# Kernel optimization log

Measured on AMD Instinct MI355X. Metric: run time of the kernel, lower is better.

The kernel has to match this reference:

```python
import jax, jax.numpy as jnp
import numpy as np

B, H, W, C = 4, 64, 64, 128  # input feature map; num_heads == filters == C


def setup_inputs() -> dict:
    key = jax.random.key(0)
    ks = jax.random.split(key, 5)
    x = jax.random.normal(ks[0], (B, H, W, C), dtype=jnp.float32)
    scale = 0.02  # keep QK^T logits in a sane range for softmax
    Wf = jax.random.normal(ks[1], (C, C), dtype=jnp.float32) * scale
    Wg = jax.random.normal(ks[2], (C, C), dtype=jnp.float32) * scale
    Wh = jax.random.normal(ks[3], (C, C), dtype=jnp.float32) * scale
    Wv = jax.random.normal(ks[4], (C, C), dtype=jnp.float32) * scale
    zeros = jnp.zeros((C,), dtype=jnp.float32)
    return {
        "x": x,
        "Wf": Wf, "bf": zeros,
        "Wg": Wg, "bg": zeros,
        "Wh": Wh, "bh": zeros,
        "Wv": Wv, "bv": zeros,
        "gamma": jnp.float32(0.01),
    }


def reference(x, Wf, bf, Wg, bg, Wh, bh, Wv, bv, gamma):
    b, h, w, c = x.shape
    n = h * w
    xf = x.reshape(b, n, c)  # 1x1 conv == per-pixel linear
    f = xf @ Wf + bf  # [b, n, heads]
    g = xf @ Wg + bg
    v = xf @ Wh + bh
    # full spatial self-attention, unscaled logits (as in the original)
    s = jnp.einsum("bnc,bmc->bnm", f, g)  # [b, n, n]
    att = jax.nn.softmax(s, axis=-1)
    ctx = jnp.einsum("bnm,bmc->bnc", att, v)  # [b, n, heads]
    ctx = gamma * ctx
    # 1x1 conv v (linear activation) + residual
    o = ctx @ Wv + bv + xf
    return o.reshape(b, h, w, -1)
```

## Files before the change

### kernel.cpp

```cpp
#include <hip/hip_runtime.h>
#include <hip/hip_bf16.h>


typedef __hip_bfloat16 bf16;
typedef unsigned char u8;
typedef unsigned int  u32;
typedef unsigned long long u64;
typedef float  floatx4 __attribute__((ext_vector_type(4)));
typedef short  shortx8 __attribute__((ext_vector_type(8)));
typedef short  shortx4 __attribute__((ext_vector_type(4)));
typedef u32    uintx4  __attribute__((ext_vector_type(4)));

#define CDIM 128
#define NROW 16384
#define NPB  4096
#define LDW  136
#define LDK  72
#define LDG8 144
#define LDV8 80
#define QTILE 128
#define NKT  64

__device__ __forceinline__ short f2bf(float v) {
    union { __hip_bfloat16 h; short s; } u; u.h = __float2bfloat16(v); return u.s;
}
__device__ __forceinline__ float bf2f(short s) {
    union { short s2; __hip_bfloat16 h; } u; u.s2 = s; return __bfloat162float(u.h);
}
__device__ __forceinline__ u8 f2fp8(float v) {
    int p = __builtin_amdgcn_cvt_pk_fp8_f32(v, v, 0, false);
    return (u8)(p & 0xff);
}
__device__ __forceinline__ u32 f2fp8x4(float a, float b, float c, float d) {
    int w = __builtin_amdgcn_cvt_pk_fp8_f32(a, b, 0, false);
    w = __builtin_amdgcn_cvt_pk_fp8_f32(c, d, w, true);
    return (u32)w;
}

__global__ __launch_bounds__(256) void proj3_kernel(
    const float* __restrict__ x,
    const float* __restrict__ Wf, const float* __restrict__ bf_,
    const float* __restrict__ Wg, const float* __restrict__ bg_,
    const float* __restrict__ Wh, const float* __restrict__ bh_,
    u8* __restrict__ f8, u8* __restrict__ g8, u8* __restrict__ vT8)
{
    __shared__ bf16 wt[128 * LDW];

    const int t    = threadIdx.x;
    const int wave = t >> 6, lane = t & 63;
    const int quad = lane >> 4, l16 = lane & 15;
    const int mtx    = blockIdx.x >> 8;
    const int rowblk = (blockIdx.x & 255) * 64;
    const int row    = rowblk + wave * 16 + l16;

    const float* Ws[3] = {Wf, Wg, Wh};
    const float* Bs[3] = {bf_, bg_, bh_};
    const float* W    = Ws[mtx];
    const float* bias = Bs[mtx];

    for (int i = t; i < 128 * 32; i += 256) {
        int k = i >> 5, n0 = (i & 31) * 4;
        floatx4 wv = *(const floatx4*)(W + k * CDIM + n0);
#pragma unroll
        for (int j = 0; j < 4; ++j)
            *(short*)&wt[(n0 + j) * LDW + k] = f2bf(wv[j]);
    }

    shortx8 afr[4];
    {
        const float* xp = x + (size_t)row * CDIM + quad * 8;
#pragma unroll
        for (int kc = 0; kc < 4; ++kc) {
            floatx4 u = *(const floatx4*)(xp + kc * 32);
            floatx4 w = *(const floatx4*)(xp + kc * 32 + 4);
            shortx8 a;
            a[0]=f2bf(u[0]); a[1]=f2bf(u[1]); a[2]=f2bf(u[2]); a[3]=f2bf(u[3]);
            a[4]=f2bf(w[0]); a[5]=f2bf(w[1]); a[6]=f2bf(w[2]); a[7]=f2bf(w[3]);
            afr[kc] = a;
        }
    }
    __syncthreads();

    floatx4 acc[8];
#pragma unroll
    for (int nt = 0; nt < 8; ++nt) acc[nt] = (floatx4){0.f, 0.f, 0.f, 0.f};
#pragma unroll
    for (int nt = 0; nt < 8; ++nt) {
        const bf16* wrow = &wt[(nt * 16 + l16) * LDW + quad * 8];
#pragma unroll
        for (int kc = 0; kc < 4; ++kc) {
            shortx8 b = *(const shortx8*)(wrow + kc * 32);
            acc[nt] = __builtin_amdgcn_mfma_f32_16x16x32_bf16(afr[kc], b, acc[nt], 0, 0, 0);
        }
    }

    if (mtx < 2) {
        u8* dst = (mtx == 0) ? f8 : g8;
#pragma unroll
        for (int nt = 0; nt < 8; ++nt) {
            int col = nt * 16 + l16;
            float bv_ = bias[col];
#pragma unroll
            for (int r = 0; r < 4; ++r) {
                int orow = rowblk + wave * 16 + quad * 4 + r;
                dst[(size_t)orow * CDIM + col] = f2fp8(acc[nt][r] + bv_);
            }
        }
    } else {
        __syncthreads();
        u8* vt8 = (u8*)wt;
        const int nloc0 = wave * 16 + quad * 4;
#pragma unroll
        for (int nt = 0; nt < 8; ++nt) {
            int ch = nt * 16 + l16;
            float bv_ = bias[ch];
            *(u32*)&vt8[ch * LDV8 + nloc0] =
                f2fp8x4(acc[nt][0] + bv_, acc[nt][1] + bv_,
                        acc[nt][2] + bv_, acc[nt][3] + bv_);
        }
        __syncthreads();
        const int ch  = t >> 1;
        const int off = (t & 1) * 32;
        const int batch = rowblk >> 12;
        const int n0 = (rowblk & 4095) + off;
        u8* dst = &vT8[((size_t)batch * CDIM + ch) * NPB + n0];
        const u8* src = &vt8[ch * LDV8 + off];
#pragma unroll
        for (int j = 0; j < 2; ++j)
            *(uintx4*)(dst + j * 16) = *(const uintx4*)(src + j * 16);
    }
}

__global__ __launch_bounds__(256, 3) void attn_kernel(
    const u8* __restrict__ f8, const u8* __restrict__ g8,
    const u8* __restrict__ vT8,
    bf16* __restrict__ Opart, float* __restrict__ lbuf, int nsplit)
{
    __shared__ u8 gs8[64 * LDG8];
    __shared__ u8 vs8[128 * LDV8];
    __shared__ u8 ps8[4 * 32 * LDV8];

    const int t    = threadIdx.x;
    const int wave = t >> 6, lane = t & 63;
    const int quad = lane >> 4, l16 = lane & 15;
    const int qg    = blockIdx.x;
    const int split = blockIdx.y;
    const int b  = qg >> 5;
    const int qt = qg & 31;
    const int qbase = b * NPB + qt * QTILE + wave * 32;

    const int kt0 = (split * NKT) / nsplit;
    const int kt1 = ((split + 1) * NKT) / nsplit;

    u64 qf[2][4];
#pragma unroll
    for (int sub = 0; sub < 2; ++sub) {
        const u8* qp = f8 + (size_t)(qbase + sub * 16 + l16) * CDIM + quad * 8;
#pragma unroll
        for (int kc = 0; kc < 4; ++kc) qf[sub][kc] = *(const u64*)(qp + kc * 32);
    }

    floatx4 o[2][8];
#pragma unroll
    for (int sub = 0; sub < 2; ++sub)
#pragma unroll
        for (int ct = 0; ct < 8; ++ct) o[sub][ct] = (floatx4){0.f, 0.f, 0.f, 0.f};
    float lacc[2][4];
#pragma unroll
    for (int sub = 0; sub < 2; ++sub)
#pragma unroll
        for (int r = 0; r < 4; ++r) lacc[sub][r] = 0.f;

    const u8* gptr = g8 + (size_t)b * NPB * CDIM;
    const u8* vptr = vT8 + (size_t)b * CDIM * NPB;

    const int gk = t >> 2, go = (t & 3) * 32;
    const int vch = t >> 1, vo = (t & 1) * 32;

    shortx8 gx[2], vx[2];
#pragma unroll
    for (int i = 0; i < 2; ++i) {
        gx[i] = *(const shortx8*)&gptr[(size_t)(kt0 * 64 + gk) * CDIM + go + i * 16];
        vx[i] = *(const shortx8*)&vptr[(size_t)vch * NPB + kt0 * 64 + vo + i * 16];
    }

    for (int kt = kt0; kt < kt1; ++kt) {
        __syncthreads();
#pragma unroll
        for (int i = 0; i < 2; ++i) {
            *(shortx8*)&gs8[gk * LDG8 + go + i * 16] = gx[i];
            *(shortx8*)&vs8[vch * LDV8 + vo + i * 16] = vx[i];
        }
        if (kt + 1 < kt1) {
            const int ktn = kt + 1;
#pragma unroll
            for (int i = 0; i < 2; ++i) {
                gx[i] = *(const shortx8*)&gptr[(size_t)(ktn * 64 + gk) * CDIM + go + i * 16];
                vx[i] = *(const shortx8*)&vptr[(size_t)vch * NPB + ktn * 64 + vo + i * 16];
            }
        }
        __syncthreads();

        floatx4 s[2][4];
#pragma unroll
        for (int sub = 0; sub < 2; ++sub)
#pragma unroll
            for (int nt = 0; nt < 4; ++nt) s[sub][nt] = (floatx4){0.f, 0.f, 0.f, 0.f};
#pragma unroll
        for (int nt = 0; nt < 4; ++nt) {
            const u8* grow = &gs8[(nt * 16 + l16) * LDG8 + quad * 8];
#pragma unroll
            for (int kc = 0; kc < 4; ++kc) {
                u64 gfr = *(const u64*)(grow + kc * 32);
                s[0][nt] = __builtin_amdgcn_mfma_f32_16x16x32_fp8_fp8(
                    (long)qf[0][kc], (long)gfr, s[0][nt], 0, 0, 0);
                s[1][nt] = __builtin_amdgcn_mfma_f32_16x16x32_fp8_fp8(
                    (long)qf[1][kc], (long)gfr, s[1][nt], 0, 0, 0);
            }
        }

#pragma unroll
        for (int sub = 0; sub < 2; ++sub) {
            u8* pw = &ps8[(wave * 32 + sub * 16 + quad * 4) * LDV8];
#pragma unroll
            for (int r = 0; r < 4; ++r) {
#pragma unroll
                for (int nt = 0; nt < 4; ++nt) {
                    float p = __expf(s[sub][nt][r]);
                    pw[r * LDV8 + nt * 16 + l16] = f2fp8(p);
                    lacc[sub][r] += p;
                }
            }
        }

        u64 pa[2][2];
#pragma unroll
        for (int sub = 0; sub < 2; ++sub) {
            const u8* pr = &ps8[(wave * 32 + sub * 16 + l16) * LDV8 + quad * 8];
            pa[sub][0] = *(const u64*)pr;
            pa[sub][1] = *(const u64*)(pr + 32);
        }

#pragma unroll
        for (int ct = 0; ct < 8; ++ct) {
            const u8* vrow = &vs8[(ct * 16 + l16) * LDV8 + quad * 8];
#pragma unroll
            for (int kc2 = 0; kc2 < 2; ++kc2) {
                u64 vfr = *(const u64*)(vrow + kc2 * 32);
                o[0][ct] = __builtin_amdgcn_mfma_f32_16x16x32_fp8_fp8(
                    (long)pa[0][kc2], (long)vfr, o[0][ct], 0, 0, 0);
                o[1][ct] = __builtin_amdgcn_mfma_f32_16x16x32_fp8_fp8(
                    (long)pa[1][kc2], (long)vfr, o[1][ct], 0, 0, 0);
            }
        }
    }

    const size_t pbase = ((size_t)qg * nsplit + split) * QTILE * CDIM;
#pragma unroll
    for (int sub = 0; sub < 2; ++sub)
#pragma unroll
        for (int ct = 0; ct < 8; ++ct) {
            int col = ct * 16 + l16;
#pragma unroll
            for (int r = 0; r < 4; ++r) {
                int rl = wave * 32 + sub * 16 + quad * 4 + r;
                *(short*)&Opart[pbase + (size_t)rl * CDIM + col] = f2bf(o[sub][ct][r]);
            }
        }
    float* lb = lbuf + ((size_t)qg * nsplit + split) * QTILE;
#pragma unroll
    for (int sub = 0; sub < 2; ++sub)
#pragma unroll
        for (int r = 0; r < 4; ++r) {
            float v = lacc[sub][r];
            v += __shfl_xor(v, 1);
            v += __shfl_xor(v, 2);
            v += __shfl_xor(v, 4);
            v += __shfl_xor(v, 8);
            if (l16 == 0) lb[wave * 32 + sub * 16 + quad * 4 + r] = v;
        }
}

__global__ __launch_bounds__(256) void out_kernel(
    const bf16* __restrict__ Opart, const float* __restrict__ lbuf,
    const float* __restrict__ Wv, const float* __restrict__ bv,
    const float* __restrict__ x, const float* __restrict__ gamma,
    float* __restrict__ out, int nsplit)
{
    __shared__ bf16 wt[128 * LDW];

    const int t    = threadIdx.x;
    const int wave = t >> 6, lane = t & 63;
    const int quad = lane >> 4, l16 = lane & 15;
    const int rowblk = blockIdx.x * 64;
    const int row    = rowblk + wave * 16 + l16;

    const float gm = gamma[0];
    for (int i = t; i < 128 * 32; i += 256) {
        int k = i >> 5, n0 = (i & 31) * 4;
        floatx4 wv4 = *(const floatx4*)(Wv + k * CDIM + n0);
#pragma unroll
        for (int j = 0; j < 4; ++j)
            *(short*)&wt[(n0 + j) * LDW + k] = f2bf(wv4[j] * gm);
    }

    const int qg = row >> 7, rl = row & 127;
    float L = 0.f;
    for (int s = 0; s < nsplit; ++s)
        L += lbuf[((size_t)qg * nsplit + s) * QTILE + rl];
    const float inv = 1.0f / L;

    shortx8 afr[4];
#pragma unroll
    for (int kc = 0; kc < 4; ++kc) {
        float a8[8] = {0,0,0,0,0,0,0,0};
        for (int s = 0; s < nsplit; ++s) {
            const bf16* p = &Opart[(((size_t)qg * nsplit + s) * QTILE + rl) * CDIM + quad * 8 + kc * 32];
            shortx8 v = *(const shortx8*)p;
#pragma unroll
            for (int j = 0; j < 8; ++j) a8[j] += bf2f(v[j]);
        }
        shortx8 a;
#pragma unroll
        for (int j = 0; j < 8; ++j) a[j] = f2bf(a8[j] * inv);
        afr[kc] = a;
    }
    __syncthreads();

    floatx4 acc[8];
#pragma unroll
    for (int nt = 0; nt < 8; ++nt) acc[nt] = (floatx4){0.f, 0.f, 0.f, 0.f};
#pragma unroll
    for (int nt = 0; nt < 8; ++nt) {
        const bf16* wrow = &wt[(nt * 16 + l16) * LDW + quad * 8];
#pragma unroll
        for (int kc = 0; kc < 4; ++kc) {
            shortx8 b = *(const shortx8*)(wrow + kc * 32);
            acc[nt] = __builtin_amdgcn_mfma_f32_16x16x32_bf16(afr[kc], b, acc[nt], 0, 0, 0);
        }
    }

#pragma unroll
    for (int nt = 0; nt < 8; ++nt) {
        int col = nt * 16 + l16;
        float bias = bv[col];
#pragma unroll
        for (int r = 0; r < 4; ++r) {
            int orow = rowblk + wave * 16 + quad * 4 + r;
            size_t idx = (size_t)orow * CDIM + col;
            out[idx] = acc[nt][r] + bias + x[idx];
        }
    }
}

extern "C" void kernel_launch(void* const* d_in, const int* in_sizes, int n_in,
                              void* d_out, int out_size, void* d_ws, size_t ws_size,
                              hipStream_t stream)
{
    const float* x   = (const float*)d_in[0];
    const float* Wf  = (const float*)d_in[1];
    const float* bf_ = (const float*)d_in[2];
    const float* Wg  = (const float*)d_in[3];
    const float* bg_ = (const float*)d_in[4];
    const float* Wh  = (const float*)d_in[5];
    const float* bh_ = (const float*)d_in[6];
    const float* Wv  = (const float*)d_in[7];
    const float* bv  = (const float*)d_in[8];
    const float* gm  = (const float*)d_in[9];
    float* out = (float*)d_out;

    const size_t need6 = (size_t)3 * NROW * CDIM
                       + (size_t)128 * 6 * QTILE * CDIM * 2
                       + (size_t)128 * 6 * QTILE * 4;
    const int nsplit = (ws_size >= need6) ? 6 : 4;

    u8*   f8    = (u8*)d_ws;
    u8*   g8    = f8 + (size_t)NROW * CDIM;
    u8*   vT8   = g8 + (size_t)NROW * CDIM;
    bf16* Opart = (bf16*)(vT8 + (size_t)NROW * CDIM);
    float* lbuf = (float*)(Opart + (size_t)128 * nsplit * QTILE * CDIM);

    proj3_kernel<<<768, 256, 0, stream>>>(x, Wf, bf_, Wg, bg_, Wh, bh_, f8, g8, vT8);
    attn_kernel<<<dim3(128, nsplit), 256, 0, stream>>>(f8, g8, vT8, Opart, lbuf, nsplit);
    out_kernel<<<256, 256, 0, stream>>>(Opart, lbuf, Wv, bv, x, gm, out, nsplit);
}
```

Before: 147.6 us.

## Store attention partials in fp8 and pack softmax probabilities via transposed QK MFMA

Swaps the QK^T MFMA operands so each lane holds four consecutive key columns for one query row. This lets the exp'd probabilities be packed four at a time into a single 32-bit fp8 LDS store, and lets the row-sum reduction use two cross-quad shuffles instead of four. The per-split partial outputs are also written as fp8 scaled by 1/8 instead of bf16, halving the intermediate traffic between the attention and output kernels. In exchange the partial context loses precision, and the fixed scale risks fp8 range or precision problems. The smaller buffer requirement can also turn on the 6-way split in more workspace configurations.

```diff
diff --git a/kernel.cpp b/kernel.cpp
--- a/kernel.cpp
+++ b/kernel.cpp
@@ -20,6 +20,7 @@
 #define LDV8 80
 #define QTILE 128
 #define NKT  64
+#define OSCALE 0.125f
 
 __device__ __forceinline__ short f2bf(float v) {
     union { __hip_bfloat16 h; short s; } u; u.h = __float2bfloat16(v); return u.s;
@@ -134,7 +135,7 @@
 __global__ __launch_bounds__(256, 3) void attn_kernel(
     const u8* __restrict__ f8, const u8* __restrict__ g8,
     const u8* __restrict__ vT8,
-    bf16* __restrict__ Opart, float* __restrict__ lbuf, int nsplit)
+    u8* __restrict__ Opart8, float* __restrict__ lbuf, int nsplit)
 {
     __shared__ u8 gs8[64 * LDG8];
     __shared__ u8 vs8[128 * LDV8];
@@ -165,11 +166,7 @@
     for (int sub = 0; sub < 2; ++sub)
 #pragma unroll
         for (int ct = 0; ct < 8; ++ct) o[sub][ct] = (floatx4){0.f, 0.f, 0.f, 0.f};
-    float lacc[2][4];
-#pragma unroll
-    for (int sub = 0; sub < 2; ++sub)
-#pragma unroll
-        for (int r = 0; r < 4; ++r) lacc[sub][r] = 0.f;
+    float lacc[2] = {0.f, 0.f};
 
     const u8* gptr = g8 + (size_t)b * NPB * CDIM;
     const u8* vptr = vT8 + (size_t)b * CDIM * NPB;
@@ -213,23 +210,23 @@
             for (int kc = 0; kc < 4; ++kc) {
                 u64 gfr = *(const u64*)(grow + kc * 32);
                 s[0][nt] = __builtin_amdgcn_mfma_f32_16x16x32_fp8_fp8(
-                    (long)qf[0][kc], (long)gfr, s[0][nt], 0, 0, 0);
+                    (long)gfr, (long)qf[0][kc], s[0][nt], 0, 0, 0);
                 s[1][nt] = __builtin_amdgcn_mfma_f32_16x16x32_fp8_fp8(
-                    (long)qf[1][kc], (long)gfr, s[1][nt], 0, 0, 0);
+                    (long)gfr, (long)qf[1][kc], s[1][nt], 0, 0, 0);
             }
         }
 
 #pragma unroll
         for (int sub = 0; sub < 2; ++sub) {
-            u8* pw = &ps8[(wave * 32 + sub * 16 + quad * 4) * LDV8];
-#pragma unroll
-            for (int r = 0; r < 4; ++r) {
-#pragma unroll
-                for (int nt = 0; nt < 4; ++nt) {
-                    float p = __expf(s[sub][nt][r]);
-                    pw[r * LDV8 + nt * 16 + l16] = f2fp8(p);
-                    lacc[sub][r] += p;
-                }
+            u8* pw = &ps8[(wave * 32 + sub * 16 + l16) * LDV8 + quad * 4];
+#pragma unroll
+            for (int nt = 0; nt < 4; ++nt) {
+                float p0 = __expf(s[sub][nt][0]);
+                float p1 = __expf(s[sub][nt][1]);
+                float p2 = __expf(s[sub][nt][2]);
+                float p3 = __expf(s[sub][nt][3]);
+                lacc[sub] += (p0 + p1) + (p2 + p3);
+                *(u32*)&pw[nt * 16] = f2fp8x4(p0, p1, p2, p3);
             }
         }
 
@@ -264,25 +261,21 @@
 #pragma unroll
             for (int r = 0; r < 4; ++r) {
                 int rl = wave * 32 + sub * 16 + quad * 4 + r;
-                *(short*)&Opart[pbase + (size_t)rl * CDIM + col] = f2bf(o[sub][ct][r]);
+                Opart8[pbase + (size_t)rl * CDIM + col] = f2fp8(o[sub][ct][r] * OSCALE);
             }
         }
     float* lb = lbuf + ((size_t)qg * nsplit + split) * QTILE;
 #pragma unroll
-    for (int sub = 0; sub < 2; ++sub)
-#pragma unroll
-        for (int r = 0; r < 4; ++r) {
-            float v = lacc[sub][r];
-            v += __shfl_xor(v, 1);
-            v += __shfl_xor(v, 2);
-            v += __shfl_xor(v, 4);
-            v += __shfl_xor(v, 8);
-            if (l16 == 0) lb[wave * 32 + sub * 16 + quad * 4 + r] = v;
-        }
+    for (int sub = 0; sub < 2; ++sub) {
+        float v = lacc[sub];
+        v += __shfl_xor(v, 16);
+        v += __shfl_xor(v, 32);
+        if (quad == 0) lb[wave * 32 + sub * 16 + l16] = v;
+    }
 }
 
 __global__ __launch_bounds__(256) void out_kernel(
-    const bf16* __restrict__ Opart, const float* __restrict__ lbuf,
+    const u8* __restrict__ Opart8, const float* __restrict__ lbuf,
     const float* __restrict__ Wv, const float* __restrict__ bv,
     const float* __restrict__ x, const float* __restrict__ gamma,
     float* __restrict__ out, int nsplit)
@@ -308,17 +301,24 @@
     float L = 0.f;
     for (int s = 0; s < nsplit; ++s)
         L += lbuf[((size_t)qg * nsplit + s) * QTILE + rl];
-    const float inv = 1.0f / L;
+    const float inv = 8.0f / L;
 
     shortx8 afr[4];
 #pragma unroll
     for (int kc = 0; kc < 4; ++kc) {
         float a8[8] = {0,0,0,0,0,0,0,0};
         for (int s = 0; s < nsplit; ++s) {
-            const bf16* p = &Opart[(((size_t)qg * nsplit + s) * QTILE + rl) * CDIM + quad * 8 + kc * 32];
-            shortx8 v = *(const shortx8*)p;
-#pragma unroll
-            for (int j = 0; j < 8; ++j) a8[j] += bf2f(v[j]);
+            const u8* p = &Opart8[(((size_t)qg * nsplit + s) * QTILE + rl) * CDIM + quad * 8 + kc * 32];
+            u32 lo = *(const u32*)p;
+            u32 hi = *(const u32*)(p + 4);
+            a8[0] += __builtin_amdgcn_cvt_f32_fp8(lo, 0);
+            a8[1] += __builtin_amdgcn_cvt_f32_fp8(lo, 1);
+            a8[2] += __builtin_amdgcn_cvt_f32_fp8(lo, 2);
+            a8[3] += __builtin_amdgcn_cvt_f32_fp8(lo, 3);
+            a8[4] += __builtin_amdgcn_cvt_f32_fp8(hi, 0);
+            a8[5] += __builtin_amdgcn_cvt_f32_fp8(hi, 1);
+            a8[6] += __builtin_amdgcn_cvt_f32_fp8(hi, 2);
+            a8[7] += __builtin_amdgcn_cvt_f32_fp8(hi, 3);
         }
         shortx8 a;
 #pragma unroll
@@ -370,17 +370,17 @@
     float* out = (float*)d_out;
 
     const size_t need6 = (size_t)3 * NROW * CDIM
-                       + (size_t)128 * 6 * QTILE * CDIM * 2
+                       + (size_t)128 * 6 * QTILE * CDIM
                        + (size_t)128 * 6 * QTILE * 4;
     const int nsplit = (ws_size >= need6) ? 6 : 4;
 
     u8*   f8    = (u8*)d_ws;
     u8*   g8    = f8 + (size_t)NROW * CDIM;
     u8*   vT8   = g8 + (size_t)NROW * CDIM;
-    bf16* Opart = (bf16*)(vT8 + (size_t)NROW * CDIM);
-    float* lbuf = (float*)(Opart + (size_t)128 * nsplit * QTILE * CDIM);
+    u8*   Opart8 = vT8 + (size_t)NROW * CDIM;
+    float* lbuf = (float*)(Opart8 + (size_t)128 * nsplit * QTILE * CDIM);
 
     proj3_kernel<<<768, 256, 0, stream>>>(x, Wf, bf_, Wg, bg_, Wh, bh_, f8, g8, vT8);
-    attn_kernel<<<dim3(128, nsplit), 256, 0, stream>>>(f8, g8, vT8, Opart, lbuf, nsplit);
-    out_kernel<<<256, 256, 0, stream>>>(Opart, lbuf, Wv, bv, x, gm, out, nsplit);
-}
+    attn_kernel<<<dim3(128, nsplit), 256, 0, stream>>>(f8, g8, vT8, Opart8, lbuf, nsplit);
+    out_kernel<<<256, 256, 0, stream>>>(Opart8, lbuf, Wv, bv, x, gm, out, nsplit);
+}
```

New measurement: 142.6 us. 1.04x faster.
